# Performance work log

Hardware: AMD Instinct MI355X
Metric: run time of the kernel (lower is better)

## Reference

```python
import jax, jax.numpy as jnp
import numpy as np

GRID = (32, 512, 512)  # volumetric query grid

def _fade(t):
    # quintic fade: 6t^5 - 15t^4 + 10t^3
    return t * t * t * (t * (t * 6.0 - 15.0) + 10.0)

def _lerp(a, b, t):
    return a + t * (b - a)

def _hash(perm, *indices):
    # chained permutation-table lookup: r = perm[(r + idx) % 256]
    r = jnp.zeros_like(indices[0])
    for idx in indices:
        r = perm[(r + idx) % 256]
    return r

def setup_inputs() -> dict:
    key = jax.random.key(0)
    kx, ky, kz = jax.random.split(key, 3)
    # coordinates uniform in [0, 64) so many lattice cells are covered
    x = jax.random.uniform(kx, GRID, dtype=jnp.float32) * 64.0
    y = jax.random.uniform(ky, GRID, dtype=jnp.float32) * 64.0
    z = jax.random.uniform(kz, GRID, dtype=jnp.float32) * 64.0
    rng = np.random.default_rng(0)
    perm = jnp.asarray(rng.permutation(256), dtype=jnp.int32)
    grad3 = jnp.asarray([
        [1, 1, 0], [-1, 1, 0], [1, -1, 0], [-1, -1, 0],
        [1, 0, 1], [-1, 0, 1], [1, 0, -1], [-1, 0, -1],
        [0, 1, 1], [0, -1, 1], [0, 1, -1], [0, -1, -1]], dtype=jnp.float32)
    return {"x": x, "y": y, "z": z, "perm": perm, "grad3": grad3}

def reference(x, y, z, perm, grad3):
    fx, fy, fz = jnp.floor(x), jnp.floor(y), jnp.floor(z)
    xi = fx.astype(jnp.int32) & 255
    yi = fy.astype(jnp.int32) & 255
    zi = fz.astype(jnp.int32) & 255
    xf, yf, zf = x - fx, y - fy, z - fz
    u, v, w = _fade(xf), _fade(yf), _fade(zf)

    aaa = _hash(perm, xi, yi, zi) % 12
    aab = _hash(perm, xi, yi, zi + 1) % 12
    aba = _hash(perm, xi, yi + 1, zi) % 12
    abb = _hash(perm, xi, yi + 1, zi + 1) % 12
    baa = _hash(perm, xi + 1, yi, zi) % 12
    bab = _hash(perm, xi + 1, yi, zi + 1) % 12
    bba = _hash(perm, xi + 1, yi + 1, zi) % 12
    bbb = _hash(perm, xi + 1, yi + 1, zi + 1) % 12

    def dot3(gi, dx, dy, dz):
        g = grad3[gi]  # gather [..., 3]
        return g[..., 0] * dx + g[..., 1] * dy + g[..., 2] * dz

    g_aaa = dot3(aaa, xf, yf, zf)
    g_aab = dot3(aab, xf, yf, zf - 1)
    g_aba = dot3(aba, xf, yf - 1, zf)
    g_abb = dot3(abb, xf, yf - 1, zf - 1)
    g_baa = dot3(baa, xf - 1, yf, zf)
    g_bab = dot3(bab, xf - 1, yf, zf - 1)
    g_bba = dot3(bba, xf - 1, yf - 1, zf)
    g_bbb = dot3(bbb, xf - 1, yf - 1, zf - 1)

    x1 = _lerp(g_aaa, g_baa, u)
    x2 = _lerp(g_aba, g_bba, u)
    x3 = _lerp(g_aab, g_bab, u)
    x4 = _lerp(g_abb, g_bbb, u)
    y1 = _lerp(x1, x2, v)
    y2 = _lerp(x3, x4, v)
    return _lerp(y1, y2, w)
```

## Files before the change

kernel.cpp:

```cpp
#include <hip/hip_runtime.h>

#define TPB 256
#define NBLOCKS 2048
#define REPL 16

__device__ __forceinline__ float fade_f(float t) {
    return t * t * t * fmaf(t, fmaf(t, 6.0f, -15.0f), 10.0f);
}

__device__ __forceinline__ float lerp_f(float a, float b, float t) {
    return fmaf(t, b - a, a);
}

__device__ __forceinline__ float gdot_w(unsigned w, float dx, float dy, float dz) {
    unsigned gi = w & 0x3Fu;
    float c1 = (gi < 8u) ? dx : dy;
    float c2 = (gi < 4u) ? dy : dz;
    unsigned s1 = w << 31;
    unsigned s2 = (w << 30) & 0x80000000u;
    return __uint_as_float(__float_as_uint(c1) ^ s1)
         + __uint_as_float(__float_as_uint(c2) ^ s2);
}

__global__ __launch_bounds__(TPB, 8) void perlin_kernel(
    const float* __restrict__ xg, const float* __restrict__ yg,
    const float* __restrict__ zg, const int* __restrict__ perm,
    float* __restrict__ out, int nquads)
{
    __shared__ unsigned T[256 * REPL];

    for (int s = threadIdx.x; s < 256 * REPL; s += TPB) {
        unsigned pv = (unsigned)perm[s >> 4];
        T[s] = (pv << 6) | (pv % 12u);
    }
    __syncthreads();

    const char* Tl = (const char*)T + ((threadIdx.x & (REPL - 1)) << 2);

    const float4* x4 = (const float4*)xg;
    const float4* y4 = (const float4*)yg;
    const float4* z4 = (const float4*)zg;
    float4* o4 = (float4*)out;

    const int stride = gridDim.x * TPB;
    for (int q = blockIdx.x * TPB + threadIdx.x; q < nquads; q += stride) {
        float4 xv = x4[q], yv = y4[q], zv = z4[q];
        float xa[4] = {xv.x, xv.y, xv.z, xv.w};
        float ya[4] = {yv.x, yv.y, yv.z, yv.w};
        float za[4] = {zv.x, zv.y, zv.z, zv.w};
        float4 res;
        float* rp = &res.x;

        #pragma unroll
        for (int e = 0; e < 4; ++e) {
            float X = xa[e], Y = ya[e], Z = za[e];
            float fx = floorf(X), fy = floorf(Y), fz = floorf(Z);
            float xf = X - fx, yf = Y - fy, zf = Z - fz;
            unsigned x6 = ((unsigned)(int)fx << 6) & 0x3FC0u;
            unsigned y6 = ((unsigned)(int)fy << 6);
            unsigned z6 = ((unsigned)(int)fz << 6);
            float u = fade_f(xf), v = fade_f(yf), w = fade_f(zf);
            float xf1 = xf - 1.0f, yf1 = yf - 1.0f, zf1 = zf - 1.0f;

            #define LK(off) (*(const unsigned*)(Tl + ((off) & 0x3FC0u)))
            unsigned A  = LK(x6),          B  = LK(x6 + 64);
            unsigned aa = LK(A + y6),      ab = LK(A + y6 + 64);
            unsigned ba = LK(B + y6),      bb = LK(B + y6 + 64);
            unsigned waaa = LK(aa + z6),   waab = LK(aa + z6 + 64);
            unsigned waba = LK(ab + z6),   wabb = LK(ab + z6 + 64);
            unsigned wbaa = LK(ba + z6),   wbab = LK(ba + z6 + 64);
            unsigned wbba = LK(bb + z6),   wbbb = LK(bb + z6 + 64);
            #undef LK

            float g_aaa = gdot_w(waaa, xf,  yf,  zf);
            float g_aab = gdot_w(waab, xf,  yf,  zf1);
            float g_aba = gdot_w(waba, xf,  yf1, zf);
            float g_abb = gdot_w(wabb, xf,  yf1, zf1);
            float g_baa = gdot_w(wbaa, xf1, yf,  zf);
            float g_bab = gdot_w(wbab, xf1, yf,  zf1);
            float g_bba = gdot_w(wbba, xf1, yf1, zf);
            float g_bbb = gdot_w(wbbb, xf1, yf1, zf1);

            float l1 = lerp_f(g_aaa, g_baa, u);
            float l2 = lerp_f(g_aba, g_bba, u);
            float l3 = lerp_f(g_aab, g_bab, u);
            float l4 = lerp_f(g_abb, g_bbb, u);
            float m1 = lerp_f(l1, l2, v);
            float m2 = lerp_f(l3, l4, v);
            rp[e] = lerp_f(m1, m2, w);
        }
        o4[q] = res;
    }
}

extern "C" void kernel_launch(void* const* d_in, const int* in_sizes, int n_in,
                              void* d_out, int out_size, void* d_ws, size_t ws_size,
                              hipStream_t stream) {
    const float* x   = (const float*)d_in[0];
    const float* y   = (const float*)d_in[1];
    const float* z   = (const float*)d_in[2];
    const int* perm  = (const int*)d_in[3];
    float* out = (float*)d_out;
    int nquads = out_size >> 2;
    perlin_kernel<<<NBLOCKS, TPB, 0, stream>>>(x, y, z, perm, out, nquads);
}
```

Baseline: 141.6 us.

## Pack adjacent permutation entries into uint2 to halve shared-memory lookups

Each shared-memory table entry now holds perm[i] and perm[i+1] together as a uint2, pre-shifted by 7 bits. One 8-byte LDS read then gives both neighbouring hash values, so each sample needs 7 lookups instead of 14. The block size also doubles to 512 threads with half as many blocks. In exchange the LDS table doubles to 32 KB per block, which may limit occupancy, and 64-bit LDS reads may bank-conflict differently.

New measurement: 141.9 us. About the same (+0.2%).

```diff
diff --git a/kernel.cpp b/kernel.cpp
--- a/kernel.cpp
+++ b/kernel.cpp
@@ -1,7 +1,7 @@
 #include <hip/hip_runtime.h>
 
-#define TPB 256
-#define NBLOCKS 2048
+#define TPB 512
+#define NBLOCKS 1024
 #define REPL 16
 
 __device__ __forceinline__ float fade_f(float t) {
@@ -13,7 +13,7 @@
 }
 
 __device__ __forceinline__ float gdot_w(unsigned w, float dx, float dy, float dz) {
-    unsigned gi = w & 0x3Fu;
+    unsigned gi = w & 0xFu;
     float c1 = (gi < 8u) ? dx : dy;
     float c2 = (gi < 4u) ? dy : dz;
     unsigned s1 = w << 31;
@@ -27,15 +27,17 @@
     const float* __restrict__ zg, const int* __restrict__ perm,
     float* __restrict__ out, int nquads)
 {
-    __shared__ unsigned T[256 * REPL];
+    __shared__ uint2 P[256 * REPL];
 
     for (int s = threadIdx.x; s < 256 * REPL; s += TPB) {
-        unsigned pv = (unsigned)perm[s >> 4];
-        T[s] = (pv << 6) | (pv % 12u);
+        int i = s >> 4;
+        unsigned p0 = (unsigned)perm[i];
+        unsigned p1 = (unsigned)perm[(i + 1) & 255];
+        P[s] = make_uint2((p0 << 7) | (p0 % 12u), (p1 << 7) | (p1 % 12u));
     }
     __syncthreads();
 
-    const char* Tl = (const char*)T + ((threadIdx.x & (REPL - 1)) << 2);
+    const char* Tl = (const char*)P + ((threadIdx.x & (REPL - 1)) << 3);
 
     const float4* x4 = (const float4*)xg;
     const float4* y4 = (const float4*)yg;
@@ -56,30 +58,30 @@
             float X = xa[e], Y = ya[e], Z = za[e];
             float fx = floorf(X), fy = floorf(Y), fz = floorf(Z);
             float xf = X - fx, yf = Y - fy, zf = Z - fz;
-            unsigned x6 = ((unsigned)(int)fx << 6) & 0x3FC0u;
-            unsigned y6 = ((unsigned)(int)fy << 6);
-            unsigned z6 = ((unsigned)(int)fz << 6);
+            unsigned x7 = (unsigned)(int)fx << 7;
+            unsigned y7 = (unsigned)(int)fy << 7;
+            unsigned z7 = (unsigned)(int)fz << 7;
             float u = fade_f(xf), v = fade_f(yf), w = fade_f(zf);
             float xf1 = xf - 1.0f, yf1 = yf - 1.0f, zf1 = zf - 1.0f;
 
-            #define LK(off) (*(const unsigned*)(Tl + ((off) & 0x3FC0u)))
-            unsigned A  = LK(x6),          B  = LK(x6 + 64);
-            unsigned aa = LK(A + y6),      ab = LK(A + y6 + 64);
-            unsigned ba = LK(B + y6),      bb = LK(B + y6 + 64);
-            unsigned waaa = LK(aa + z6),   waab = LK(aa + z6 + 64);
-            unsigned waba = LK(ab + z6),   wabb = LK(ab + z6 + 64);
-            unsigned wbaa = LK(ba + z6),   wbab = LK(ba + z6 + 64);
-            unsigned wbba = LK(bb + z6),   wbbb = LK(bb + z6 + 64);
+            #define LK(t) (*(const uint2*)(Tl + ((t) & 0x7F80u)))
+            uint2 lv1 = LK(x7);
+            uint2 p_a = LK(lv1.x + y7);
+            uint2 p_b = LK(lv1.y + y7);
+            uint2 paa = LK(p_a.x + z7);
+            uint2 pab = LK(p_a.y + z7);
+            uint2 pba = LK(p_b.x + z7);
+            uint2 pbb = LK(p_b.y + z7);
             #undef LK
 
-            float g_aaa = gdot_w(waaa, xf,  yf,  zf);
-            float g_aab = gdot_w(waab, xf,  yf,  zf1);
-            float g_aba = gdot_w(waba, xf,  yf1, zf);
-            float g_abb = gdot_w(wabb, xf,  yf1, zf1);
-            float g_baa = gdot_w(wbaa, xf1, yf,  zf);
-            float g_bab = gdot_w(wbab, xf1, yf,  zf1);
-            float g_bba = gdot_w(wbba, xf1, yf1, zf);
-            float g_bbb = gdot_w(wbbb, xf1, yf1, zf1);
+            float g_aaa = gdot_w(paa.x, xf,  yf,  zf);
+            float g_aab = gdot_w(paa.y, xf,  yf,  zf1);
+            float g_aba = gdot_w(pab.x, xf,  yf1, zf);
+            float g_abb = gdot_w(pab.y, xf,  yf1, zf1);
+            float g_baa = gdot_w(pba.x, xf1, yf,  zf);
+            float g_bab = gdot_w(pba.y, xf1, yf,  zf1);
+            float g_bba = gdot_w(pbb.x, xf1, yf1, zf);
+            float g_bbb = gdot_w(pbb.y, xf1, yf1, zf1);
 
             float l1 = lerp_f(g_aaa, g_baa, u);
             float l2 = lerp_f(g_aba, g_bba, u);
```
